# Optimization experiments

Hardware: AMD Instinct MI355X
Metric: run time of the kernel (lower is better)

## Reference

```python
import jax, jax.numpy as jnp
import numpy as np

N, E, D, T = 10000, 320000, 128, 128


def _layer_norm(x, g, b, eps=1e-5):
    mu = jnp.mean(x, axis=-1, keepdims=True)
    var = jnp.mean(jnp.square(x - mu), axis=-1, keepdims=True)
    return (x - mu) * jax.lax.rsqrt(var + eps) * g + b


def setup_inputs() -> dict:
    key = jax.random.key(0)
    ks = jax.random.split(key, 24)
    s = 0.05

    def lin(k, fin, fout):
        k1, k2 = jax.random.split(k)
        return (jax.random.normal(k1, (fin, fout), jnp.float32) * s,
                jax.random.normal(k2, (fout,), jnp.float32) * s)

    W_tp, b_tp = lin(ks[5], T, D)
    W_sg, b_sg = lin(ks[6], D, D)
    W_dg, b_dg = lin(ks[7], D, D)
    W_eg, b_eg = lin(ks[8], D, D)
    W_su, b_su = lin(ks[9], D, D)
    W_du, b_du = lin(ks[10], D, D)
    return {
        'node_feats': jax.random.normal(ks[0], (N, D), jnp.float32),
        'edge_feats': jax.random.normal(ks[1], (E, D), jnp.float32),
        'time_feats': jax.random.normal(ks[2], (N, T), jnp.float32),
        'src': jax.random.randint(ks[3], (E,), 0, N),
        'dst': jax.random.randint(ks[4], (E,), 0, N),
        'W_tp': W_tp, 'b_tp': b_tp,
        'W_sg': W_sg, 'b_sg': b_sg,
        'W_dg': W_dg, 'b_dg': b_dg,
        'W_eg': W_eg, 'b_eg': b_eg,
        'W_su': W_su, 'b_su': b_su,
        'W_du': W_du, 'b_du': b_du,
        'ln_e_g': jnp.ones((D,), jnp.float32), 'ln_e_b': jnp.zeros((D,), jnp.float32),
        'ln_n_g': jnp.ones((D,), jnp.float32), 'ln_n_b': jnp.zeros((D,), jnp.float32),
    }


def reference(node_feats, edge_feats, time_feats, src, dst,
              W_tp, b_tp, W_sg, b_sg, W_dg, b_dg, W_eg, b_eg,
              W_su, b_su, W_du, b_du, ln_e_g, ln_e_b, ln_n_g, ln_n_b):
    n_nodes = node_feats.shape[0]
    # per-node gate projections (time proj folded into source gate)
    e_src = node_feats @ W_sg + b_sg + time_feats @ W_tp + b_tp   # [N, D]
    e_dst = node_feats @ W_dg + b_dg                              # [N, D]
    # edge gating: gather from both endpoints + edge feature projection
    m = e_src[src] + e_dst[dst] + edge_feats @ W_eg + b_eg        # [E, D]
    sigma = jax.nn.sigmoid(m)                                     # [E, D]
    # gated message passing: scatter-add over destination nodes
    Bh = node_feats @ W_du + b_du                                 # [N, D]
    sum_sigma_h = jax.ops.segment_sum(Bh[src] * sigma, dst, num_segments=n_nodes)
    sum_sigma = jax.ops.segment_sum(sigma, dst, num_segments=n_nodes)
    h = sum_sigma_h / (sum_sigma + 1e-6)                          # [N, D]
    x = node_feats @ W_su + b_su + h
    x = jax.nn.silu(_layer_norm(x, ln_n_g, ln_n_b))
    y = jax.nn.silu(_layer_norm(m, ln_e_g, ln_e_b))
    x = node_feats + x  # residual
    y = edge_feats + y
    return (x, y)
```

## Files before the change

kernel.cpp:

```cpp
#include <hip/hip_runtime.h>
#include <hip/hip_bf16.h>

#define N_NODES 10000
#define N_EDGES 320000
#define D 128
#define NBINS 10000

typedef float f32x4 __attribute__((ext_vector_type(4)));
typedef float f32x2 __attribute__((ext_vector_type(2)));
typedef short bf16x8 __attribute__((ext_vector_type(8)));
typedef short bf16x16 __attribute__((ext_vector_type(16)));

static __device__ inline short f2bf(float f) {
    union { __hip_bfloat16 h; short s; } u;
    u.h = __float2bfloat16(f);
    return u.s;
}

static __device__ inline float bf2f(short s) {
    union { float f; unsigned u; } x;
    x.u = ((unsigned)(unsigned short)s) << 16;
    return x.f;
}

static __device__ inline float fast_rcp(float x) { return __builtin_amdgcn_rcpf(x); }

__global__ void prep_hist(const float* __restrict__ W_sg, const float* __restrict__ W_tp,
                          const float* __restrict__ W_dg, const float* __restrict__ W_du,
                          const float* __restrict__ W_su, const float* __restrict__ W_eg,
                          short* __restrict__ Wsrc, short* __restrict__ Wdg,
                          short* __restrict__ Wdu, short* __restrict__ Wsu,
                          short* __restrict__ Weg,
                          const int* __restrict__ dst, int* __restrict__ cnt) {
    int bid = blockIdx.x;
    if (bid < 1250) {
        int i = bid * 256 + threadIdx.x;
        atomicAdd(&cnt[dst[i]], 1);
        return;
    }
    int idx = (bid - 1250) * 256 + threadIdx.x;
    const float* W0; const float* W1; short* out; int i2;
    if (idx < 32768)      { W0 = W_sg; W1 = W_tp; out = Wsrc; i2 = idx; }
    else if (idx < 49152) { W0 = W_dg; W1 = W_dg; out = Wdg;  i2 = idx - 32768; }
    else if (idx < 65536) { W0 = W_du; W1 = W_du; out = Wdu;  i2 = idx - 49152; }
    else if (idx < 81920) { W0 = W_su; W1 = W_su; out = Wsu;  i2 = idx - 65536; }
    else                  { W0 = W_eg; W1 = W_eg; out = Weg;  i2 = idx - 81920; }
    int b  = i2 & 7;
    int l  = (i2 >> 3) & 63;
    int jt = (i2 >> 9) & 7;
    int t  = i2 >> 12;
    int k = 32 * t + ((l >> 4) * 8) + b;
    int j = jt * 16 + (l & 15);
    float v = (k < 128) ? W0[k * 128 + j] : W1[(k - 128) * 128 + j];
    out[i2] = f2bf(v);
}

__launch_bounds__(1024)
__global__ void scan_kernel(const int* __restrict__ cnt, int* __restrict__ cursor) {
    __shared__ int s[1024];
    int t = threadIdx.x;
    int b0 = t * 10;
    int loc[10];
    int tot = 0;
#pragma unroll
    for (int i = 0; i < 10; ++i) {
        int v = (b0 + i < NBINS) ? cnt[b0 + i] : 0;
        loc[i] = tot; tot += v;
    }
    s[t] = tot;
    __syncthreads();
    for (int off = 1; off < 1024; off <<= 1) {
        int v = (t >= off) ? s[t - off] : 0;
        __syncthreads();
        s[t] += v;
        __syncthreads();
    }
    int base = (t == 0) ? 0 : s[t - 1];
#pragma unroll
    for (int i = 0; i < 10; ++i)
        if (b0 + i < NBINS) cursor[b0 + i] = base + loc[i];
}

__global__ void scatter_kernel(const int* __restrict__ src, const int* __restrict__ dst,
                               int* __restrict__ cursor,
                               int* __restrict__ perm,
                               int* __restrict__ src_s, int* __restrict__ dst_s) {
    int i = blockIdx.x * 256 + threadIdx.x;
    if (i < N_EDGES) {
        int d = dst[i];
        int p = atomicAdd(&cursor[d], 1);
        perm[p] = i;
        src_s[p] = src[i];
        dst_s[p] = d;
    }
}

__launch_bounds__(256)
__global__ void node_proj_kernel(const float* __restrict__ node,
                                 const float* __restrict__ timef,
                                 const short* __restrict__ Wsrc_pk,
                                 const short* __restrict__ Wdg_pk,
                                 const short* __restrict__ Wdu_pk,
                                 const short* __restrict__ Wsu_pk,
                                 const float* __restrict__ b_sg, const float* __restrict__ b_tp,
                                 const float* __restrict__ b_dg, const float* __restrict__ b_du,
                                 const float* __restrict__ b_su, const float* __restrict__ b_eg,
                                 short* __restrict__ spk,
                                 short* __restrict__ dpk,
                                 float* __restrict__ xs,
                                 float* __restrict__ ss, float* __restrict__ ssh) {
    {
        int r0b = blockIdx.x * 64;
        int nrows = N_NODES - r0b; if (nrows > 64) nrows = 64;
        f32x4 z = {0.f, 0.f, 0.f, 0.f};
        f32x4* s4 = (f32x4*)(ss + (size_t)r0b * D);
        f32x4* h4 = (f32x4*)(ssh + (size_t)r0b * D);
        int nch = nrows * D / 4;
        for (int i = threadIdx.x; i < nch; i += 256) { s4[i] = z; h4[i] = z; }
    }

    int tid = threadIdx.x;
    int w = tid >> 6;
    int l = tid & 63;
    int g = l >> 4;
    int lr = l & 15;
    int r0 = blockIdx.x * 64 + w * 16;
    int arow = r0 + lr;

    bf16x8 aN[4], aT[4];
    if (arow < N_NODES) {
        const float* np = node + (size_t)arow * D;
        const float* tp = timef + (size_t)arow * D;
#pragma unroll
        for (int t = 0; t < 4; ++t) {
            int k0 = 32 * t + g * 8;
            f32x4 v0 = *(const f32x4*)(np + k0);
            f32x4 v1 = *(const f32x4*)(np + k0 + 4);
            f32x4 u0 = *(const f32x4*)(tp + k0);
            f32x4 u1 = *(const f32x4*)(tp + k0 + 4);
            bf16x8 a, b;
#pragma unroll
            for (int i = 0; i < 4; ++i) {
                a[i] = f2bf(v0[i]); a[4 + i] = f2bf(v1[i]);
                b[i] = f2bf(u0[i]); b[4 + i] = f2bf(u1[i]);
            }
            aN[t] = a; aT[t] = b;
        }
    } else {
        bf16x8 z = {0, 0, 0, 0, 0, 0, 0, 0};
#pragma unroll
        for (int t = 0; t < 4; ++t) { aN[t] = z; aT[t] = z; }
    }

    const bf16x8* Bsrc = (const bf16x8*)Wsrc_pk;
    const bf16x8* Bdg  = (const bf16x8*)Wdg_pk;
    const bf16x8* Bdu  = (const bf16x8*)Wdu_pk;
    const bf16x8* Bsu  = (const bf16x8*)Wsu_pk;

    {
        bf16x8 chunk[4];
#pragma unroll
        for (int jt = 0; jt < 8; ++jt) {
            int c = jt * 16 + lr;
            f32x4 acc = {0.f, 0.f, 0.f, 0.f};
#pragma unroll
            for (int t = 0; t < 4; ++t)
                acc = __builtin_amdgcn_mfma_f32_16x16x32_bf16(aN[t], Bsrc[(t * 8 + jt) * 64 + l], acc, 0, 0, 0);
#pragma unroll
            for (int t = 0; t < 4; ++t)
                acc = __builtin_amdgcn_mfma_f32_16x16x32_bf16(aT[t], Bsrc[((4 + t) * 8 + jt) * 64 + l], acc, 0, 0, 0);
            float bias = b_sg[c] + b_tp[c];
#pragma unroll
            for (int r = 0; r < 4; ++r) chunk[r][jt] = f2bf(acc[r] + bias);
        }
#pragma unroll
        for (int r = 0; r < 4; ++r) {
            int row = r0 + g * 4 + r;
            if (row < N_NODES) *(bf16x8*)(spk + (size_t)row * 256 + lr * 16) = chunk[r];
        }
    }

    {
        bf16x8 chD[4], chH[4];
        float xsv[4][8];
#pragma unroll
        for (int jt = 0; jt < 8; ++jt) {
            int c = jt * 16 + lr;
            f32x4 a0 = {0.f, 0.f, 0.f, 0.f}, a1 = a0, a2 = a0;
#pragma unroll
            for (int t = 0; t < 4; ++t) {
                a0 = __builtin_amdgcn_mfma_f32_16x16x32_bf16(aN[t], Bdg[(t * 8 + jt) * 64 + l], a0, 0, 0, 0);
                a1 = __builtin_amdgcn_mfma_f32_16x16x32_bf16(aN[t], Bdu[(t * 8 + jt) * 64 + l], a1, 0, 0, 0);
                a2 = __builtin_amdgcn_mfma_f32_16x16x32_bf16(aN[t], Bsu[(t * 8 + jt) * 64 + l], a2, 0, 0, 0);
            }
            float bdgc = b_dg[c] + b_eg[c];
            float bdu = b_du[c], bsu = b_su[c];
#pragma unroll
            for (int r = 0; r < 4; ++r) {
                chD[r][jt] = f2bf(a0[r] + bdgc);
                chH[r][jt] = f2bf(a1[r] + bdu);
                xsv[r][jt] = a2[r] + bsu;
            }
        }
#pragma unroll
        for (int r = 0; r < 4; ++r) {
            int row = r0 + g * 4 + r;
            if (row < N_NODES) {
                *(bf16x8*)(dpk + (size_t)row * D + lr * 8) = chD[r];
                *(bf16x8*)(spk + (size_t)row * 256 + lr * 16 + 8) = chH[r];
#pragma unroll
                for (int jt = 0; jt < 8; ++jt)
                    xs[(size_t)row * D + jt * 16 + lr] = xsv[r][jt];
            }
        }
    }
}


#define TILE_LOAD_IDX(S, E0) \
    const int eA##S = perm[(E0) + lr]; \
    int eidx##S[4], sidx##S[4], didx##S[4]; \
    _Pragma("unroll") \
    for (int r = 0; r < 4; ++r) { \
        int p = (E0) + g * 4 + r; \
        eidx##S[r] = perm[p]; sidx##S[r] = src_s[p]; didx##S[r] = dst_s[p]; \
    } \
    const int df##S = __shfl(didx##S[0], 0); \
    const bool uni##S = (df##S == __shfl(didx##S[3], 48));

#define TILE_GATHER(S) \
    bf16x16 esbh##S[4]; bf16x8 edv##S[4]; \
    _Pragma("unroll") \
    for (int r = 0; r < 4; ++r) \
        esbh##S[r] = *(const bf16x16*)(spk + (size_t)sidx##S[r] * 256 + lr * 16); \
    edv##S[0] = *(const bf16x8*)(dpk + (size_t)didx##S[0] * D + lr * 8); \
    if (!uni##S) { \
        _Pragma("unroll") \
        for (int r = 1; r < 4; ++r) \
            edv##S[r] = *(const bf16x8*)(dpk + (size_t)didx##S[r] * D + lr * 8); \
    } else { edv##S[1] = edv##S[0]; edv##S[2] = edv##S[0]; edv##S[3] = edv##S[0]; }

#define TILE_AFRAG(S) \
    bf16x8 aE##S[4]; \
    { const float* ep = edgef + (size_t)eA##S * D; \
      _Pragma("unroll") \
      for (int t = 0; t < 4; ++t) { \
        int k0 = 32 * t + g * 8; \
        f32x4 v0 = *(const f32x4*)(ep + k0); \
        f32x4 v1 = *(const f32x4*)(ep + k0 + 4); \
        bf16x8 a; \
        _Pragma("unroll") \
        for (int i = 0; i < 4; ++i) { a[i] = f2bf(v0[i]); a[4 + i] = f2bf(v1[i]); } \
        aE##S[t] = a; } }

#define TILE_COMPUTE(S) \
    f32x4 acc##S[8]; \
    _Pragma("unroll") \
    for (int jt = 0; jt < 8; ++jt) { \
        f32x4 c4 = {0.f, 0.f, 0.f, 0.f}; \
        _Pragma("unroll") \
        for (int t = 0; t < 4; ++t) \
            c4 = __builtin_amdgcn_mfma_f32_16x16x32_bf16(aE##S[t], Bp[(t * 8 + jt) * 64 + l], c4, 0, 0, 0); \
        acc##S[jt] = c4; } \
    float sum##S[4] = {0.f, 0.f, 0.f, 0.f}, sq##S[4] = {0.f, 0.f, 0.f, 0.f}; \
    _Pragma("unroll") \
    for (int jt = 0; jt < 8; ++jt) { \
        int c = jt * 16 + lr; \
        float sg[4], bsg[4]; \
        _Pragma("unroll") \
        for (int r = 0; r < 4; ++r) { \
            float m = acc##S[jt][r] + bf2f(esbh##S[r][jt]) + bf2f(edv##S[r][jt]); \
            acc##S[jt][r] = m; \
            float s = fast_rcp(1.f + __expf(-m)); \
            sg[r] = s; bsg[r] = bf2f(esbh##S[r][8 + jt]) * s; \
            sum##S[r] += m; sq##S[r] += m * m; } \
        if (uni##S) { \
            float aS = (sg[0] + sg[1]) + (sg[2] + sg[3]); \
            float aH = (bsg[0] + bsg[1]) + (bsg[2] + bsg[3]); \
            aS += __shfl_xor(aS, 16); aH += __shfl_xor(aH, 16); \
            aS += __shfl_xor(aS, 32); aH += __shfl_xor(aH, 32); \
            if (g == 0) { \
                atomicAdd(&ss [(size_t)df##S * D + c], aS); \
                atomicAdd(&ssh[(size_t)df##S * D + c], aH); } \
        } else { \
            float aS = sg[0], aH = bsg[0]; \
            _Pragma("unroll") \
            for (int r = 1; r < 4; ++r) { \
                if (didx##S[r] == didx##S[r - 1]) { aS += sg[r]; aH += bsg[r]; } \
                else { \
                    atomicAdd(&ss [(size_t)didx##S[r - 1] * D + c], aS); \
                    atomicAdd(&ssh[(size_t)didx##S[r - 1] * D + c], aH); \
                    aS = sg[r]; aH = bsg[r]; } } \
            atomicAdd(&ss [(size_t)didx##S[3] * D + c], aS); \
            atomicAdd(&ssh[(size_t)didx##S[3] * D + c], aH); } }

#define TILE_EPILOGUE(S) \
    _Pragma("unroll") \
    for (int r = 0; r < 4; ++r) { \
        float s = sum##S[r], q = sq##S[r]; \
        _Pragma("unroll") \
        for (int mk = 1; mk < 16; mk <<= 1) { s += __shfl_xor(s, mk); q += __shfl_xor(q, mk); } \
        float mean = s * (1.f / D); \
        sum##S[r] = mean; \
        sq##S[r] = rsqrtf(q * (1.f / D) - mean * mean + 1e-5f); } \
    _Pragma("unroll") \
    for (int jt = 0; jt < 8; ++jt) { \
        int c = jt * 16 + lr; \
        float gc = ln_g[c], bc = ln_b[c]; \
        _Pragma("unroll") \
        for (int r = 0; r < 4; ++r) { \
            float v = (acc##S[jt][r] - sum##S[r]) * sq##S[r] * gc + bc; \
            float sl = v * fast_rcp(1.f + __expf(-v)); \
            size_t off = (size_t)eidx##S[r] * D + c; \
            y[off] = __builtin_nontemporal_load(&edgef[off]) + sl; } }

__launch_bounds__(256)
__global__ void edge_kernel(const float* __restrict__ edgef,
                            const int* __restrict__ perm,
                            const int* __restrict__ src_s, const int* __restrict__ dst_s,
                            const short* __restrict__ Weg_pk,
                            const short* __restrict__ spk,
                            const short* __restrict__ dpk,
                            const float* __restrict__ ln_g, const float* __restrict__ ln_b,
                            float* __restrict__ ss, float* __restrict__ ssh,
                            float* __restrict__ y) {
    __shared__ short Bs[128 * 128];
    {
        const bf16x8* gw = (const bf16x8*)Weg_pk;
        bf16x8* sw = (bf16x8*)Bs;
        for (int i = threadIdx.x; i < 2048; i += 256) sw[i] = gw[i];
    }
    __syncthreads();

    int tid = threadIdx.x;
    int w = tid >> 6;
    int l = tid & 63;
    int g = l >> 4;
    int lr = l & 15;

    int b = blockIdx.x;
    const int q = 312, rr = 4;
    int xcd = b & 7, boff = b >> 3;
    int swz = (xcd < rr ? xcd * (q + 1) : rr * (q + 1) + (xcd - rr) * q) + boff;
    int ebase = swz * 128 + w * 32;

    const bf16x8* Bp = (const bf16x8*)Bs;

    TILE_LOAD_IDX(0, ebase)
    TILE_LOAD_IDX(1, ebase + 16)
    TILE_GATHER(0)
    TILE_AFRAG(0)
    TILE_AFRAG(1)
    TILE_COMPUTE(0)
    TILE_GATHER(1)
    TILE_EPILOGUE(0)
    TILE_COMPUTE(1)
    TILE_EPILOGUE(1)
}

__launch_bounds__(256)
__global__ void node_out_kernel(const float* __restrict__ node,
                                const float* __restrict__ xs,
                                const float* __restrict__ ssh, const float* __restrict__ ss,
                                const float* __restrict__ ln_g, const float* __restrict__ ln_b,
                                float* __restrict__ x) {
    int w = threadIdx.x >> 6;
    int l = threadIdx.x & 63;
    int row = blockIdx.x * 4 + w;
    if (row >= N_NODES) return;
    size_t base = (size_t)row * D + 2 * l;
    f32x2 xv = *(const f32x2*)(xs + base);
    f32x2 hs = *(const f32x2*)(ssh + base);
    f32x2 sv = *(const f32x2*)(ss + base);
    float v0 = xv[0] + hs[0] / (sv[0] + 1e-6f);
    float v1 = xv[1] + hs[1] / (sv[1] + 1e-6f);
    float s = v0 + v1, q = v0 * v0 + v1 * v1;
#pragma unroll
    for (int mk = 1; mk < 64; mk <<= 1) { s += __shfl_xor(s, mk); q += __shfl_xor(q, mk); }
    float mean = s * (1.f / D);
    float var = q * (1.f / D) - mean * mean;
    float rstd = rsqrtf(var + 1e-5f);
    float t0 = (v0 - mean) * rstd * ln_g[2 * l] + ln_b[2 * l];
    float t1 = (v1 - mean) * rstd * ln_g[2 * l + 1] + ln_b[2 * l + 1];
    t0 = t0 * fast_rcp(1.f + __expf(-t0));
    t1 = t1 * fast_rcp(1.f + __expf(-t1));
    f32x2 nv = *(const f32x2*)(node + base);
    f32x2 outv;
    outv[0] = nv[0] + t0;
    outv[1] = nv[1] + t1;
    *(f32x2*)(x + base) = outv;
}

extern "C" void kernel_launch(void* const* d_in, const int* in_sizes, int n_in,
                              void* d_out, int out_size, void* d_ws, size_t ws_size,
                              hipStream_t stream) {
    const float* node  = (const float*)d_in[0];
    const float* edgef = (const float*)d_in[1];
    const float* timef = (const float*)d_in[2];
    const int*   src   = (const int*)d_in[3];
    const int*   dst   = (const int*)d_in[4];
    const float* W_tp = (const float*)d_in[5];  const float* b_tp = (const float*)d_in[6];
    const float* W_sg = (const float*)d_in[7];  const float* b_sg = (const float*)d_in[8];
    const float* W_dg = (const float*)d_in[9];  const float* b_dg = (const float*)d_in[10];
    const float* W_eg = (const float*)d_in[11]; const float* b_eg = (const float*)d_in[12];
    const float* W_su = (const float*)d_in[13]; const float* b_su = (const float*)d_in[14];
    const float* W_du = (const float*)d_in[15]; const float* b_du = (const float*)d_in[16];
    const float* ln_e_g = (const float*)d_in[17]; const float* ln_e_b = (const float*)d_in[18];
    const float* ln_n_g = (const float*)d_in[19]; const float* ln_n_b = (const float*)d_in[20];

    char* ws = (char*)d_ws;
    size_t nd = (size_t)N_NODES * D;
    float* ss    = (float*)ws; ws += nd * 4;
    float* ssh   = (float*)ws; ws += nd * 4;
    float* xs    = (float*)ws; ws += nd * 4;
    short* spk   = (short*)ws; ws += (size_t)N_NODES * 256 * 2;
    short* dpk   = (short*)ws; ws += nd * 2;
    short* Wsrc_pk = (short*)ws; ws += 256 * 128 * 2;
    short* Wdg_pk  = (short*)ws; ws += 128 * 128 * 2;
    short* Wdu_pk  = (short*)ws; ws += 128 * 128 * 2;
    short* Wsu_pk  = (short*)ws; ws += 128 * 128 * 2;
    short* Weg_pk  = (short*)ws; ws += 128 * 128 * 2;
    int* cnt       = (int*)ws; ws += 10240 * 4;
    int* cursor    = (int*)ws; ws += 10240 * 4;
    int* perm      = (int*)ws; ws += (size_t)N_EDGES * 4;
    int* src_s     = (int*)ws; ws += (size_t)N_EDGES * 4;
    int* dst_s     = (int*)ws; ws += (size_t)N_EDGES * 4;

    hipMemsetAsync(cnt, 0, 10240 * 4, stream);

    prep_hist<<<1634, 256, 0, stream>>>(W_sg, W_tp, W_dg, W_du, W_su, W_eg,
                                        Wsrc_pk, Wdg_pk, Wdu_pk, Wsu_pk, Weg_pk,
                                        dst, cnt);
    scan_kernel<<<1, 1024, 0, stream>>>(cnt, cursor);
    scatter_kernel<<<(N_EDGES + 255) / 256, 256, 0, stream>>>(src, dst, cursor, perm, src_s, dst_s);

    node_proj_kernel<<<(N_NODES + 63) / 64, 256, 0, stream>>>(
        node, timef, Wsrc_pk, Wdg_pk, Wdu_pk, Wsu_pk,
        b_sg, b_tp, b_dg, b_du, b_su, b_eg, spk, dpk, xs, ss, ssh);

    edge_kernel<<<2500, 256, 0, stream>>>(
        edgef, perm, src_s, dst_s, Weg_pk, spk, dpk,
        ln_e_g, ln_e_b, ss, ssh, (float*)d_out + nd);

    node_out_kernel<<<N_NODES / 4, 256, 0, stream>>>(
        node, xs, ssh, ss, ln_n_g, ln_n_b, (float*)d_out);
}
```

Measured before the change: 256.4 us.

## Split node projection across twice the blocks, merge tile atomics, memset accumulators

The node projection kernel now launches twice as many blocks: the first half computes the source gate (node and time inputs) and the second half computes the dst/du/su projections, raising parallelism on 157-block launches. Zeroing of the ss/ssh accumulators moves from the kernel into a single larger memset alongside the histogram counters, with the workspace reordered so they are contiguous. In the edge kernel, when both 16-edge tiles of a wave share a single destination, the first tile's reductions are deferred and added to the second tile's, halving atomics. The edge-feature reload in the epilogue drops its nontemporal hint.

```diff
diff --git a/kernel.cpp b/kernel.cpp
--- a/kernel.cpp
+++ b/kernel.cpp
@@ -107,57 +107,56 @@
                                  const float* __restrict__ b_su, const float* __restrict__ b_eg,
                                  short* __restrict__ spk,
                                  short* __restrict__ dpk,
-                                 float* __restrict__ xs,
-                                 float* __restrict__ ss, float* __restrict__ ssh) {
-    {
-        int r0b = blockIdx.x * 64;
-        int nrows = N_NODES - r0b; if (nrows > 64) nrows = 64;
-        f32x4 z = {0.f, 0.f, 0.f, 0.f};
-        f32x4* s4 = (f32x4*)(ss + (size_t)r0b * D);
-        f32x4* h4 = (f32x4*)(ssh + (size_t)r0b * D);
-        int nch = nrows * D / 4;
-        for (int i = threadIdx.x; i < nch; i += 256) { s4[i] = z; h4[i] = z; }
-    }
-
+                                 float* __restrict__ xs) {
     int tid = threadIdx.x;
     int w = tid >> 6;
     int l = tid & 63;
     int g = l >> 4;
     int lr = l & 15;
-    int r0 = blockIdx.x * 64 + w * 16;
+    const bool pathB = blockIdx.x >= 157;
+    int blk = pathB ? blockIdx.x - 157 : blockIdx.x;
+    int r0 = blk * 64 + w * 16;
     int arow = r0 + lr;
 
-    bf16x8 aN[4], aT[4];
+    bf16x8 aN[4];
     if (arow < N_NODES) {
         const float* np = node + (size_t)arow * D;
-        const float* tp = timef + (size_t)arow * D;
 #pragma unroll
         for (int t = 0; t < 4; ++t) {
             int k0 = 32 * t + g * 8;
             f32x4 v0 = *(const f32x4*)(np + k0);
             f32x4 v1 = *(const f32x4*)(np + k0 + 4);
-            f32x4 u0 = *(const f32x4*)(tp + k0);
-            f32x4 u1 = *(const f32x4*)(tp + k0 + 4);
-            bf16x8 a, b;
-#pragma unroll
-            for (int i = 0; i < 4; ++i) {
-                a[i] = f2bf(v0[i]); a[4 + i] = f2bf(v1[i]);
-                b[i] = f2bf(u0[i]); b[4 + i] = f2bf(u1[i]);
-            }
-            aN[t] = a; aT[t] = b;
+            bf16x8 a;
+#pragma unroll
+            for (int i = 0; i < 4; ++i) { a[i] = f2bf(v0[i]); a[4 + i] = f2bf(v1[i]); }
+            aN[t] = a;
         }
     } else {
         bf16x8 z = {0, 0, 0, 0, 0, 0, 0, 0};
 #pragma unroll
-        for (int t = 0; t < 4; ++t) { aN[t] = z; aT[t] = z; }
-    }
-
-    const bf16x8* Bsrc = (const bf16x8*)Wsrc_pk;
-    const bf16x8* Bdg  = (const bf16x8*)Wdg_pk;
-    const bf16x8* Bdu  = (const bf16x8*)Wdu_pk;
-    const bf16x8* Bsu  = (const bf16x8*)Wsu_pk;
-
-    {
+        for (int t = 0; t < 4; ++t) aN[t] = z;
+    }
+
+    if (!pathB) {
+        bf16x8 aT[4];
+        if (arow < N_NODES) {
+            const float* tp = timef + (size_t)arow * D;
+#pragma unroll
+            for (int t = 0; t < 4; ++t) {
+                int k0 = 32 * t + g * 8;
+                f32x4 u0 = *(const f32x4*)(tp + k0);
+                f32x4 u1 = *(const f32x4*)(tp + k0 + 4);
+                bf16x8 b;
+#pragma unroll
+                for (int i = 0; i < 4; ++i) { b[i] = f2bf(u0[i]); b[4 + i] = f2bf(u1[i]); }
+                aT[t] = b;
+            }
+        } else {
+            bf16x8 z = {0, 0, 0, 0, 0, 0, 0, 0};
+#pragma unroll
+            for (int t = 0; t < 4; ++t) aT[t] = z;
+        }
+        const bf16x8* Bsrc = (const bf16x8*)Wsrc_pk;
         bf16x8 chunk[4];
 #pragma unroll
         for (int jt = 0; jt < 8; ++jt) {
@@ -178,9 +177,10 @@
             int row = r0 + g * 4 + r;
             if (row < N_NODES) *(bf16x8*)(spk + (size_t)row * 256 + lr * 16) = chunk[r];
         }
-    }
-
-    {
+    } else {
+        const bf16x8* Bdg = (const bf16x8*)Wdg_pk;
+        const bf16x8* Bdu = (const bf16x8*)Wdu_pk;
+        const bf16x8* Bsu = (const bf16x8*)Wsu_pk;
         bf16x8 chD[4], chH[4];
         float xsv[4][8];
 #pragma unroll
@@ -253,7 +253,7 @@
         for (int i = 0; i < 4; ++i) { a[i] = f2bf(v0[i]); a[4 + i] = f2bf(v1[i]); } \
         aE##S[t] = a; } }
 
-#define TILE_COMPUTE(S) \
+#define TILE_COMPUTE(S, DEFER, ADDPREV) \
     f32x4 acc##S[8]; \
     _Pragma("unroll") \
     for (int jt = 0; jt < 8; ++jt) { \
@@ -279,9 +279,12 @@
             float aH = (bsg[0] + bsg[1]) + (bsg[2] + bsg[3]); \
             aS += __shfl_xor(aS, 16); aH += __shfl_xor(aH, 16); \
             aS += __shfl_xor(aS, 32); aH += __shfl_xor(aH, 32); \
-            if (g == 0) { \
-                atomicAdd(&ss [(size_t)df##S * D + c], aS); \
-                atomicAdd(&ssh[(size_t)df##S * D + c], aH); } \
+            if (DEFER && comb) { aS0[jt] = aS; aH0[jt] = aH; } \
+            else { \
+                if (ADDPREV && comb) { aS += aS0[jt]; aH += aH0[jt]; } \
+                if (g == 0) { \
+                    atomicAdd(&ss [(size_t)df##S * D + c], aS); \
+                    atomicAdd(&ssh[(size_t)df##S * D + c], aH); } } \
         } else { \
             float aS = sg[0], aH = bsg[0]; \
             _Pragma("unroll") \
@@ -312,7 +315,7 @@
             float v = (acc##S[jt][r] - sum##S[r]) * sq##S[r] * gc + bc; \
             float sl = v * fast_rcp(1.f + __expf(-v)); \
             size_t off = (size_t)eidx##S[r] * D + c; \
-            y[off] = __builtin_nontemporal_load(&edgef[off]) + sl; } }
+            y[off] = edgef[off] + sl; } }
 
 __launch_bounds__(256)
 __global__ void edge_kernel(const float* __restrict__ edgef,
@@ -348,13 +351,16 @@
 
     TILE_LOAD_IDX(0, ebase)
     TILE_LOAD_IDX(1, ebase + 16)
+    const bool comb = uni0 && uni1 && (df0 == df1);
+    float aS0[8], aH0[8];
+
     TILE_GATHER(0)
     TILE_AFRAG(0)
     TILE_AFRAG(1)
-    TILE_COMPUTE(0)
+    TILE_COMPUTE(0, 1, 0)
     TILE_GATHER(1)
     TILE_EPILOGUE(0)
-    TILE_COMPUTE(1)
+    TILE_COMPUTE(1, 0, 1)
     TILE_EPILOGUE(1)
 }
 
@@ -410,6 +416,8 @@
 
     char* ws = (char*)d_ws;
     size_t nd = (size_t)N_NODES * D;
+    int* cnt       = (int*)ws; ws += 10240 * 4;
+    int* cursor    = (int*)ws; ws += 10240 * 4;
     float* ss    = (float*)ws; ws += nd * 4;
     float* ssh   = (float*)ws; ws += nd * 4;
     float* xs    = (float*)ws; ws += nd * 4;
@@ -420,13 +428,11 @@
     short* Wdu_pk  = (short*)ws; ws += 128 * 128 * 2;
     short* Wsu_pk  = (short*)ws; ws += 128 * 128 * 2;
     short* Weg_pk  = (short*)ws; ws += 128 * 128 * 2;
-    int* cnt       = (int*)ws; ws += 10240 * 4;
-    int* cursor    = (int*)ws; ws += 10240 * 4;
     int* perm      = (int*)ws; ws += (size_t)N_EDGES * 4;
     int* src_s     = (int*)ws; ws += (size_t)N_EDGES * 4;
     int* dst_s     = (int*)ws; ws += (size_t)N_EDGES * 4;
 
-    hipMemsetAsync(cnt, 0, 10240 * 4, stream);
+    hipMemsetAsync(cnt, 0, 2 * 10240 * 4 + 2 * nd * 4, stream);
 
     prep_hist<<<1634, 256, 0, stream>>>(W_sg, W_tp, W_dg, W_du, W_su, W_eg,
                                         Wsrc_pk, Wdg_pk, Wdu_pk, Wsu_pk, Weg_pk,
@@ -434,9 +440,9 @@
     scan_kernel<<<1, 1024, 0, stream>>>(cnt, cursor);
     scatter_kernel<<<(N_EDGES + 255) / 256, 256, 0, stream>>>(src, dst, cursor, perm, src_s, dst_s);
 
-    node_proj_kernel<<<(N_NODES + 63) / 64, 256, 0, stream>>>(
+    node_proj_kernel<<<314, 256, 0, stream>>>(
         node, timef, Wsrc_pk, Wdg_pk, Wdu_pk, Wsu_pk,
-        b_sg, b_tp, b_dg, b_du, b_su, b_eg, spk, dpk, xs, ss, ssh);
+        b_sg, b_tp, b_dg, b_du, b_su, b_eg, spk, dpk, xs);
 
     edge_kernel<<<2500, 256, 0, stream>>>(
         edgef, perm, src_s, dst_s, Weg_pk, spk, dpk,
```

After: 256.8 us. About the same (+0.1%).
